# Kernel tuning notes

Measured on AMD Instinct MI355X. Metric: run time of the kernel, lower is better.

Reference implementation:

```python
import jax, jax.numpy as jnp
import numpy as np

TEMP = 0.05
GAMMA = 1.1

B, D, N = 1024, 256, 100000


def setup_inputs() -> dict:
    key = jax.random.key(0)
    k1, k2, k3 = jax.random.split(key, 3)
    inputs = jax.random.normal(k1, (B, D), dtype=jnp.float32)
    targets = jax.random.randint(k2, (B,), 0, N)
    features = jax.random.normal(k3, (N, D), dtype=jnp.float32)
    features = features / jnp.linalg.norm(features, axis=1, keepdims=True)
    return {"inputs": inputs, "targets": targets, "features": features}


def reference(inputs, targets, features):
    # F.normalize(inputs, dim=1)
    x = inputs / jnp.linalg.norm(inputs, axis=1, keepdims=True)
    # gather prototypes and cosine similarity per sample
    protos = features[targets]                      # [B, D]
    sim = jnp.sum(x * protos, axis=1)               # [B]
    # per-target min of sim (segment-min replaces the python loop over unique targets)
    seg_min = jax.ops.segment_min(sim, targets, num_segments=N)   # [N]
    threshold = jnp.clip(seg_min[targets], 0.0, None) * GAMMA      # [B]
    weight = (sim <= threshold).astype(jnp.float32)                # [B] (used only in backward update)
    # logits against full memory bank, scaled by temperature
    out = (x @ features.T) / TEMP                   # [B, N]
    return out
```

## Files before the change

### kernel.cpp

```cpp
#include <hip/hip_runtime.h>
#include <hip/hip_bf16.h>
#include <cstdint>

typedef unsigned short u16;
typedef __attribute__((ext_vector_type(8))) short short8;
typedef __attribute__((ext_vector_type(4))) float f32x4;

__device__ __forceinline__ u16 f2bf(float f) {
  unsigned u = __float_as_uint(f);
  u += 0x7fffu + ((u >> 16) & 1u);
  return (u16)(u >> 16);
}

__global__ void norm_cast_kernel(const float* __restrict__ in, u16* __restrict__ xb) {
  const int row = blockIdx.x;
  const int t = threadIdx.x;
  float v = in[row * 256 + t];
  float s = v * v;
  #pragma unroll
  for (int off = 32; off >= 1; off >>= 1) s += __shfl_xor(s, off, 64);
  __shared__ float wsum[4];
  if ((t & 63) == 0) wsum[t >> 6] = s;
  __syncthreads();
  const float tot = wsum[0] + wsum[1] + wsum[2] + wsum[3];
  xb[row * 256 + t] = f2bf(v * rsqrtf(tot));
}

__global__ void cvt_bf16_kernel(const float4* __restrict__ in, ushort4* __restrict__ out, int n4) {
  const int i = blockIdx.x * 256 + threadIdx.x;
  if (i < n4) {
    float4 v = in[i];
    out[i] = make_ushort4(f2bf(v.x), f2bf(v.y), f2bf(v.z), f2bf(v.w));
  }
}

template <bool CONVB>
__global__ __launch_bounds__(256) void gemm_kernel(
    const u16* __restrict__ A,
    const u16* __restrict__ Bbf,
    const float* __restrict__ Bfp,
    float* __restrict__ C, int Nn)
{
  __shared__ u16 As[128 * 32];
  __shared__ u16 Bs[128 * 32];

  const int tid  = threadIdx.x;
  const int wave = tid >> 6;
  const int lane = tid & 63;
  const int m0 = blockIdx.x * 128;
  const int n0 = blockIdx.y * 128;
  const int wm = (wave & 1) * 64;
  const int wn = (wave >> 1) * 64;

  f32x4 acc[4][4] = {};

  const int srow   = tid >> 2;
  const int schunk = (tid & 3) * 8;

  for (int k0 = 0; k0 < 256; k0 += 32) {
    #pragma unroll
    for (int r = 0; r < 2; ++r) {
      const u16* gp = A + (size_t)(m0 + r * 64 + srow) * 256 + k0 + schunk;
      u16* lp = (u16*)As + (r * 4 + wave) * 512;
      __builtin_amdgcn_global_load_lds(
          (const __attribute__((address_space(1))) void*)gp,
          (__attribute__((address_space(3))) void*)lp, 16, 0, 0);
    }
    if constexpr (!CONVB) {
      #pragma unroll
      for (int r = 0; r < 2; ++r) {
        int grow = n0 + r * 64 + srow;
        if (grow >= Nn) grow = Nn - 1;
        const u16* gp = Bbf + (size_t)grow * 256 + k0 + schunk;
        u16* lp = (u16*)Bs + (r * 4 + wave) * 512;
        __builtin_amdgcn_global_load_lds(
            (const __attribute__((address_space(1))) void*)gp,
            (__attribute__((address_space(3))) void*)lp, 16, 0, 0);
      }
    } else {
      #pragma unroll
      for (int r = 0; r < 4; ++r) {
        const int idx = r * 256 + tid;
        const int row = idx >> 3;
        const int kc  = (idx & 7) * 4;
        int grow = n0 + row;
        if (grow >= Nn) grow = Nn - 1;
        float4 v = *(const float4*)(Bfp + (size_t)grow * 256 + k0 + kc);
        *(ushort4*)(&Bs[row * 32 + kc]) =
            make_ushort4(f2bf(v.x), f2bf(v.y), f2bf(v.z), f2bf(v.w));
      }
    }
    __syncthreads();

    const int fr = lane & 15;
    const int kc = (lane >> 4) * 8;
    short8 af[4], bfr[4];
    #pragma unroll
    for (int i = 0; i < 4; ++i) {
      af[i]  = *(const short8*)(&As[(wm + i * 16 + fr) * 32 + kc]);
      bfr[i] = *(const short8*)(&Bs[(wn + i * 16 + fr) * 32 + kc]);
    }
    #pragma unroll
    for (int mi = 0; mi < 4; ++mi)
      #pragma unroll
      for (int ni = 0; ni < 4; ++ni)
        acc[mi][ni] = __builtin_amdgcn_mfma_f32_16x16x32_bf16(af[mi], bfr[ni], acc[mi][ni], 0, 0, 0);
    __syncthreads();
  }

  const int col   = lane & 15;
  const int rquad = (lane >> 4) * 4;
  #pragma unroll
  for (int mi = 0; mi < 4; ++mi) {
    const int m = m0 + wm + mi * 16 + rquad;
    #pragma unroll
    for (int ni = 0; ni < 4; ++ni) {
      const int n = n0 + wn + ni * 16 + col;
      if (n < Nn) {
        float* cp = C + (size_t)m * Nn + n;
        #pragma unroll
        for (int i = 0; i < 4; ++i)
          cp[(size_t)i * Nn] = acc[mi][ni][i] * 20.0f;
      }
    }
  }
}

extern "C" void kernel_launch(void* const* d_in, const int* in_sizes, int n_in,
                              void* d_out, int out_size, void* d_ws, size_t ws_size,
                              hipStream_t stream) {
  const float* inputs   = (const float*)d_in[0];
  const float* features = (const float*)d_in[2];
  float* out = (float*)d_out;

  const int Bv = in_sizes[1];
  const int Dv = in_sizes[0] / Bv;
  const int Nn = in_sizes[2] / Dv;

  u16* xb = (u16*)d_ws;
  const size_t x_bytes = ((size_t)Bv * Dv * 2 + 255) & ~(size_t)255;
  u16* fb = (u16*)((char*)d_ws + x_bytes);
  const size_t f_bytes = (size_t)Nn * Dv * 2;
  const bool fits = ws_size >= x_bytes + f_bytes;

  norm_cast_kernel<<<dim3(Bv), dim3(256), 0, stream>>>(inputs, xb);

  dim3 grid(Bv / 128, (Nn + 127) / 128);
  if (fits) {
    const int n4 = (Nn * Dv) / 4;
    cvt_bf16_kernel<<<dim3((n4 + 255) / 256), dim3(256), 0, stream>>>(
        (const float4*)features, (ushort4*)fb, n4);
    gemm_kernel<false><<<grid, dim3(256), 0, stream>>>(xb, fb, nullptr, out, Nn);
  } else {
    gemm_kernel<true><<<grid, dim3(256), 0, stream>>>(xb, nullptr, features, out, Nn);
  }
}
```

Baseline: 552.4 us.

## Stage GEMM epilogue through LDS for coalesced float4 stores and use BK=64

Doubles the K tile from 32 to 64 so each block runs four main-loop iterations with two MFMA sub-steps each, halving barriers. The output tile is staged through padded shared memory in two halves so each row is written with coalesced float4 stores instead of scattered scalar stores. The fallback path that converted fp32 features inside the GEMM is removed, so the kernel now assumes the workspace can hold the bf16 copy of features. LDS use rises to about 33 KB per block, which may lower occupancy.

```diff
diff --git a/kernel.cpp b/kernel.cpp
--- a/kernel.cpp
+++ b/kernel.cpp
@@ -34,15 +34,14 @@
   }
 }
 
-template <bool CONVB>
 __global__ __launch_bounds__(256) void gemm_kernel(
     const u16* __restrict__ A,
     const u16* __restrict__ Bbf,
-    const float* __restrict__ Bfp,
     float* __restrict__ C, int Nn)
 {
-  __shared__ u16 As[128 * 32];
-  __shared__ u16 Bs[128 * 32];
+  __shared__ char smem[64 * 132 * 4];
+  u16* As = (u16*)smem;
+  u16* Bs = (u16*)(smem + 128 * 64 * 2);
 
   const int tid  = threadIdx.x;
   const int wave = tid >> 6;
@@ -54,73 +53,79 @@
 
   f32x4 acc[4][4] = {};
 
-  const int srow   = tid >> 2;
-  const int schunk = (tid & 3) * 8;
+  const int srow   = wave * 8 + (lane >> 3);
+  const int schunk = (lane & 7) * 8;
 
-  for (int k0 = 0; k0 < 256; k0 += 32) {
+  for (int k0 = 0; k0 < 256; k0 += 64) {
     #pragma unroll
-    for (int r = 0; r < 2; ++r) {
-      const u16* gp = A + (size_t)(m0 + r * 64 + srow) * 256 + k0 + schunk;
-      u16* lp = (u16*)As + (r * 4 + wave) * 512;
-      __builtin_amdgcn_global_load_lds(
-          (const __attribute__((address_space(1))) void*)gp,
-          (__attribute__((address_space(3))) void*)lp, 16, 0, 0);
-    }
-    if constexpr (!CONVB) {
-      #pragma unroll
-      for (int r = 0; r < 2; ++r) {
-        int grow = n0 + r * 64 + srow;
-        if (grow >= Nn) grow = Nn - 1;
-        const u16* gp = Bbf + (size_t)grow * 256 + k0 + schunk;
-        u16* lp = (u16*)Bs + (r * 4 + wave) * 512;
+    for (int r = 0; r < 4; ++r) {
+      {
+        const u16* gp = A + (size_t)(m0 + r * 32 + srow) * 256 + k0 + schunk;
+        u16* lp = As + (r * 4 + wave) * 512;
         __builtin_amdgcn_global_load_lds(
             (const __attribute__((address_space(1))) void*)gp,
             (__attribute__((address_space(3))) void*)lp, 16, 0, 0);
       }
-    } else {
-      #pragma unroll
-      for (int r = 0; r < 4; ++r) {
-        const int idx = r * 256 + tid;
-        const int row = idx >> 3;
-        const int kc  = (idx & 7) * 4;
-        int grow = n0 + row;
+      {
+        int grow = n0 + r * 32 + srow;
         if (grow >= Nn) grow = Nn - 1;
-        float4 v = *(const float4*)(Bfp + (size_t)grow * 256 + k0 + kc);
-        *(ushort4*)(&Bs[row * 32 + kc]) =
-            make_ushort4(f2bf(v.x), f2bf(v.y), f2bf(v.z), f2bf(v.w));
+        const u16* gp = Bbf + (size_t)grow * 256 + k0 + schunk;
+        u16* lp = Bs + (r * 4 + wave) * 512;
+        __builtin_amdgcn_global_load_lds(
+            (const __attribute__((address_space(1))) void*)gp,
+            (__attribute__((address_space(3))) void*)lp, 16, 0, 0);
       }
     }
     __syncthreads();
 
     const int fr = lane & 15;
     const int kc = (lane >> 4) * 8;
-    short8 af[4], bfr[4];
     #pragma unroll
-    for (int i = 0; i < 4; ++i) {
-      af[i]  = *(const short8*)(&As[(wm + i * 16 + fr) * 32 + kc]);
-      bfr[i] = *(const short8*)(&Bs[(wn + i * 16 + fr) * 32 + kc]);
+    for (int kk = 0; kk < 2; ++kk) {
+      short8 af[4], bfr[4];
+      #pragma unroll
+      for (int i = 0; i < 4; ++i) {
+        af[i]  = *(const short8*)(&As[(wm + i * 16 + fr) * 64 + kk * 32 + kc]);
+        bfr[i] = *(const short8*)(&Bs[(wn + i * 16 + fr) * 64 + kk * 32 + kc]);
+      }
+      #pragma unroll
+      for (int mi = 0; mi < 4; ++mi)
+        #pragma unroll
+        for (int ni = 0; ni < 4; ++ni)
+          acc[mi][ni] = __builtin_amdgcn_mfma_f32_16x16x32_bf16(af[mi], bfr[ni], acc[mi][ni], 0, 0, 0);
     }
-    #pragma unroll
-    for (int mi = 0; mi < 4; ++mi)
-      #pragma unroll
-      for (int ni = 0; ni < 4; ++ni)
-        acc[mi][ni] = __builtin_amdgcn_mfma_f32_16x16x32_bf16(af[mi], bfr[ni], acc[mi][ni], 0, 0, 0);
     __syncthreads();
   }
 
   const int col   = lane & 15;
   const int rquad = (lane >> 4) * 4;
+  float* ep = (float*)smem;
+  const int c4    = (tid & 31) * 4;
+  const int rbase = tid >> 5;
+
   #pragma unroll
-  for (int mi = 0; mi < 4; ++mi) {
-    const int m = m0 + wm + mi * 16 + rquad;
+  for (int h = 0; h < 2; ++h) {
+    if (h) __syncthreads();
+    if (wm == h * 64) {
+      #pragma unroll
+      for (int mi = 0; mi < 4; ++mi)
+        #pragma unroll
+        for (int ni = 0; ni < 4; ++ni)
+          #pragma unroll
+          for (int i = 0; i < 4; ++i)
+            ep[(mi * 16 + rquad + i) * 132 + wn + ni * 16 + col] = acc[mi][ni][i] * 20.0f;
+    }
+    __syncthreads();
     #pragma unroll
-    for (int ni = 0; ni < 4; ++ni) {
-      const int n = n0 + wn + ni * 16 + col;
-      if (n < Nn) {
-        float* cp = C + (size_t)m * Nn + n;
-        #pragma unroll
-        for (int i = 0; i < 4; ++i)
-          cp[(size_t)i * Nn] = acc[mi][ni][i] * 20.0f;
+    for (int rr = 0; rr < 8; ++rr) {
+      const int row = rr * 8 + rbase;
+      const int gn  = n0 + c4;
+      float4 v = *(const float4*)&ep[row * 132 + c4];
+      float* cp = C + (size_t)(m0 + h * 64 + row) * Nn + gn;
+      if (gn + 4 <= Nn) {
+        *(float4*)cp = v;
+      } else {
+        for (int j = 0; gn + j < Nn; ++j) cp[j] = ((const float*)&v)[j];
       }
     }
   }
@@ -140,18 +145,13 @@
   u16* xb = (u16*)d_ws;
   const size_t x_bytes = ((size_t)Bv * Dv * 2 + 255) & ~(size_t)255;
   u16* fb = (u16*)((char*)d_ws + x_bytes);
-  const size_t f_bytes = (size_t)Nn * Dv * 2;
-  const bool fits = ws_size >= x_bytes + f_bytes;
 
   norm_cast_kernel<<<dim3(Bv), dim3(256), 0, stream>>>(inputs, xb);
 
+  const int n4 = (Nn * Dv) / 4;
+  cvt_bf16_kernel<<<dim3((n4 + 255) / 256), dim3(256), 0, stream>>>(
+      (const float4*)features, (ushort4*)fb, n4);
+
   dim3 grid(Bv / 128, (Nn + 127) / 128);
-  if (fits) {
-    const int n4 = (Nn * Dv) / 4;
-    cvt_bf16_kernel<<<dim3((n4 + 255) / 256), dim3(256), 0, stream>>>(
-        (const float4*)features, (ushort4*)fb, n4);
-    gemm_kernel<false><<<grid, dim3(256), 0, stream>>>(xb, fb, nullptr, out, Nn);
-  } else {
-    gemm_kernel<true><<<grid, dim3(256), 0, stream>>>(xb, nullptr, features, out, Nn);
-  }
+  gemm_kernel<<<grid, dim3(256), 0, stream>>>(xb, fb, out, Nn);
 }
```

After: 564.6 us. 2.2% more time.
